# Kernel tuning notes

Measured on AMD Instinct MI355X. Metric: run time of the kernel, lower is better.

## Reference

```python
import jax, jax.numpy as jnp
import numpy as np

N_NODES = 50000
N_EDGES = 1_600_000
IN_DIM = 128
OUT_DIM = 128


def setup_inputs() -> dict:
    key = jax.random.key(0)
    k1, k2, k3, k4, k5, k6 = jax.random.split(key, 6)
    H = jax.random.normal(k1, (N_NODES, IN_DIM), dtype=jnp.float32)
    edge_src = jax.random.randint(k2, (N_EDGES,), 0, N_NODES, dtype=jnp.int32)
    edge_dst = jnp.sort(jax.random.randint(k3, (N_EDGES,), 0, N_NODES, dtype=jnp.int32))
    edge_weight = jax.random.uniform(k4, (N_EDGES,), dtype=jnp.float32)
    bound = np.sqrt(6.0 / (IN_DIM + OUT_DIM))
    W = jax.random.uniform(k5, (IN_DIM, OUT_DIM), dtype=jnp.float32, minval=-bound, maxval=bound)
    b = jax.random.normal(k6, (OUT_DIM,), dtype=jnp.float32)
    return {"H": H, "edge_src": edge_src, "edge_dst": edge_dst,
            "edge_weight": edge_weight, "W": W, "b": b}


def reference(H, edge_src, edge_dst, edge_weight, W, b):
    # A_hat @ H: gather source features, scale by edge weight, scatter-sum to dst.
    msgs = edge_weight[:, None] * jnp.take(H, edge_src, axis=0)   # [E, in_dim]
    agg = jax.ops.segment_sum(msgs, edge_dst, num_segments=N_NODES)  # [N, in_dim]
    # Dense transform + bias (no activation in original forward).
    return agg @ W + b
```

## Files before the change

### kernel.cpp

```cpp
#include <hip/hip_runtime.h>

#define IN_DIM 128
#define OUT_DIM 128

typedef __attribute__((ext_vector_type(8))) short short8v;
typedef __attribute__((ext_vector_type(4))) float float4v;
typedef __attribute__((ext_vector_type(4))) unsigned int uint4v;

__device__ __forceinline__ ushort f2bf(float f) {
    unsigned int u = __builtin_bit_cast(unsigned int, f);
    unsigned int r = (u + 0x7fffu + ((u >> 16) & 1u)) >> 16;
    return (ushort)r;
}

__device__ __forceinline__ unsigned int pk2bf(float x, float y) {
#if __has_builtin(__builtin_amdgcn_cvt_pk_bf16_f32)
    typedef __attribute__((ext_vector_type(2))) __bf16 bf2;
    bf2 r = __builtin_amdgcn_cvt_pk_bf16_f32(x, y);
    return __builtin_bit_cast(unsigned int, r);
#else
    return (unsigned int)f2bf(x) | ((unsigned int)f2bf(y) << 16);
#endif
}

__global__ __launch_bounds__(256) void prep_kernel(const float* __restrict__ W,
                                                   ushort* __restrict__ Wt) {
    int k0 = blockIdx.x * 8;
    int n = threadIdx.x & 127;
    int half = threadIdx.x >> 7;
#pragma unroll
    for (int kp = 0; kp < 2; ++kp) {
        int k = k0 + (half * 2 + kp) * 2;
        float v0 = W[k * 128 + n];
        float v1 = W[(k + 1) * 128 + n];
        *(unsigned int*)&Wt[n * 136 + k] = pk2bf(v0, v1);
    }
}

__global__ __launch_bounds__(256) void gemm_kernel(const float* __restrict__ H,
                                                   const ushort* __restrict__ Wt_g,
                                                   unsigned char* __restrict__ T8,
                                                   float* __restrict__ S, int M,
                                                   const int* __restrict__ edst,
                                                   int* __restrict__ rp,
                                                   int E, int nb_gemm) {
    __shared__ ushort Ws[128 * 136];

    const int t = threadIdx.x;

    if (blockIdx.x >= nb_gemm) {
        int n = (blockIdx.x - nb_gemm) * 256 + t;
        if (n <= M) {
            int lo = 0, hi = E;
            while (lo < hi) {
                int mid = (lo + hi) >> 1;
                if (edst[mid] < n) lo = mid + 1; else hi = mid;
            }
            rp[n] = lo;
        }
        return;
    }

    const int row0 = blockIdx.x * 64;

#pragma unroll
    for (int f = t; f < 2176; f += 256)
        ((short8v*)Ws)[f] = ((const short8v*)Wt_g)[f];

    const int w = t >> 6;
    const int l = t & 63;
    const int m16 = l & 15;
    const int kq = (l >> 4) * 8;
    const int gr = row0 + w * 16 + m16;

    float4 h[8];
    if (gr < M) {
#pragma unroll
        for (int ks = 0; ks < 4; ++ks) {
            h[ks * 2]     = *(const float4*)&H[gr * 128 + ks * 32 + kq];
            h[ks * 2 + 1] = *(const float4*)&H[gr * 128 + ks * 32 + kq + 4];
        }
    } else {
#pragma unroll
        for (int i = 0; i < 8; ++i) h[i] = make_float4(0.f, 0.f, 0.f, 0.f);
    }

    short8v bfrag[4];
#pragma unroll
    for (int ks = 0; ks < 4; ++ks) {
        uint4v u;
        u[0] = pk2bf(h[ks * 2].x, h[ks * 2].y);
        u[1] = pk2bf(h[ks * 2].z, h[ks * 2].w);
        u[2] = pk2bf(h[ks * 2 + 1].x, h[ks * 2 + 1].y);
        u[3] = pk2bf(h[ks * 2 + 1].z, h[ks * 2 + 1].w);
        bfrag[ks] = __builtin_bit_cast(short8v, u);
    }

    __syncthreads();

    float4v acc[8];
#pragma unroll
    for (int nt = 0; nt < 8; ++nt) acc[nt] = (float4v){0.f, 0.f, 0.f, 0.f};

#pragma unroll
    for (int ks = 0; ks < 4; ++ks) {
#pragma unroll
        for (int nt = 0; nt < 8; ++nt) {
            short8v afrag = *(const short8v*)&Ws[(nt * 16 + m16) * 136 + ks * 32 + kq];
            acc[nt] = __builtin_amdgcn_mfma_f32_16x16x32_bf16(afrag, bfrag[ks], acc[nt], 0, 0, 0);
        }
    }

    float mx = 0.f;
#pragma unroll
    for (int nt = 0; nt < 8; ++nt) {
#pragma unroll
        for (int k = 0; k < 4; ++k) mx = fmaxf(mx, fabsf(acc[nt][k]));
    }
    mx = fmaxf(mx, __shfl_xor(mx, 16));
    mx = fmaxf(mx, __shfl_xor(mx, 32));

    const float inv = 127.0f / fmaxf(mx, 1e-20f);

    if (gr < M) {
        const int qd = l >> 4;
        if (qd == 0) S[gr] = mx * (1.0f / 127.0f);
#pragma unroll
        for (int nt = 0; nt < 8; ++nt) {
            unsigned int p = 0;
#pragma unroll
            for (int k = 0; k < 4; ++k) {
                int qi = (int)__builtin_rintf(acc[nt][k] * inv);
                qi = qi > 127 ? 127 : (qi < -127 ? -127 : qi);
                p |= ((unsigned int)qi & 0xffu) << (k * 8);
            }
            *(unsigned int*)&T8[gr * 128 + nt * 16 + qd * 4] = p;
        }
    }
}

__global__ __launch_bounds__(256) void scatter_kernel(const ushort* __restrict__ T16,
                                                      const float* __restrict__ S,
                                                      const int* __restrict__ esrc,
                                                      const float* __restrict__ ew,
                                                      const int* __restrict__ rp,
                                                      const float* __restrict__ b,
                                                      float* __restrict__ out) {
    const int node = blockIdx.x * 4 + (threadIdx.x >> 6);
    const int lane = threadIdx.x & 63;
    const int col = lane << 1;

    const int s = rp[node];
    const int e = rp[node + 1];

    float2 bias = *(const float2*)&b[col];
    float ax = bias.x, ay = bias.y;

    for (int c = s; c < e; c += 64) {
        int idx = c + lane;
        int srcl = 0;
        float wl = 0.f;
        if (idx < e) { srcl = esrc[idx]; wl = ew[idx]; }
        int wli = __builtin_bit_cast(int, wl);
        int nn = e - c;
        if (nn > 64) nn = 64;

        for (int j = 0; j < nn; j += 8) {
            int ss[8];
            float ws[8];
            ushort vv[8];
#pragma unroll
            for (int q = 0; q < 8; ++q) {
                ss[q] = __builtin_amdgcn_readlane(srcl, j + q);
                float wq = __builtin_bit_cast(float, __builtin_amdgcn_readlane(wli, j + q));
                ws[q] = wq * S[ss[q]];
            }
#pragma unroll
            for (int q = 0; q < 8; ++q)
                vv[q] = T16[(unsigned int)ss[q] * 64u + (unsigned int)lane];
#pragma unroll
            for (int q = 0; q < 8; ++q) {
                int lo8 = (int)(signed char)(vv[q] & 0xff);
                int hi8 = (int)(signed char)(vv[q] >> 8);
                ax += ws[q] * (float)lo8;
                ay += ws[q] * (float)hi8;
            }
        }
    }

    *(float2*)&out[node * 128 + col] = make_float2(ax, ay);
}

extern "C" void kernel_launch(void* const* d_in, const int* in_sizes, int n_in,
                              void* d_out, int out_size, void* d_ws, size_t ws_size,
                              hipStream_t stream) {
    const float* H    = (const float*)d_in[0];
    const int*   esrc = (const int*)d_in[1];
    const int*   edst = (const int*)d_in[2];
    const float* ew   = (const float*)d_in[3];
    const float* W    = (const float*)d_in[4];
    const float* b    = (const float*)d_in[5];
    float* out = (float*)d_out;

    const int M = in_sizes[0] / IN_DIM;
    const int E = in_sizes[1];

    unsigned char* T8 = (unsigned char*)d_ws;
    size_t off = (size_t)M * 128;
    float* S  = (float*)((char*)d_ws + off);
    off += (size_t)M * 4;
    ushort* Wt = (ushort*)((char*)d_ws + off);
    off += 128 * 136 * 2;
    int* rp = (int*)((char*)d_ws + off);

    prep_kernel<<<16, 256, 0, stream>>>(W, Wt);

    const int nb_gemm = (M + 63) / 64;
    const int nb_rp   = (M + 1 + 255) / 256;
    gemm_kernel<<<nb_gemm + nb_rp, 256, 0, stream>>>(H, Wt, T8, S, M, edst, rp, E, nb_gemm);

    scatter_kernel<<<(M + 3) / 4, 256, 0, stream>>>((const ushort*)T8, S, esrc, ew, rp, b, out);
}
```

Baseline: 144.1 us.

## Store transformed features as fp16 instead of int8 with per-row scales

The GEMM output is now stored as packed fp16 rather than int8 with a per-row scale array, which removes the row max reduction and quantization in the GEMM epilogue and the scale lookups in the scatter kernel. The scatter kernel is also restructured: it drops the wave-cooperative edge loading with readlane broadcast and loads edge indices and weights directly with uniform (readfirstlane) bounds, unrolled by 8. The cost is twice the gather traffic per edge from the intermediate table. In exchange, accuracy is better than int8.

```diff
diff --git a/kernel.cpp b/kernel.cpp
--- a/kernel.cpp
+++ b/kernel.cpp
@@ -6,6 +6,8 @@
 typedef __attribute__((ext_vector_type(8))) short short8v;
 typedef __attribute__((ext_vector_type(4))) float float4v;
 typedef __attribute__((ext_vector_type(4))) unsigned int uint4v;
+typedef __attribute__((ext_vector_type(2))) unsigned int uint2v;
+typedef __attribute__((ext_vector_type(2))) __fp16 half2v;
 
 __device__ __forceinline__ ushort f2bf(float f) {
     unsigned int u = __builtin_bit_cast(unsigned int, f);
@@ -21,6 +23,11 @@
 #else
     return (unsigned int)f2bf(x) | ((unsigned int)f2bf(y) << 16);
 #endif
+}
+
+__device__ __forceinline__ unsigned int pk2f16(float x, float y) {
+    half2v r = __builtin_amdgcn_cvt_pkrtz(x, y);
+    return __builtin_bit_cast(unsigned int, r);
 }
 
 __global__ __launch_bounds__(256) void prep_kernel(const float* __restrict__ W,
@@ -39,8 +46,8 @@
 
 __global__ __launch_bounds__(256) void gemm_kernel(const float* __restrict__ H,
                                                    const ushort* __restrict__ Wt_g,
-                                                   unsigned char* __restrict__ T8,
-                                                   float* __restrict__ S, int M,
+                                                   __fp16* __restrict__ T,
+                                                   int M,
                                                    const int* __restrict__ edst,
                                                    int* __restrict__ rp,
                                                    int E, int nb_gemm) {
@@ -111,36 +118,18 @@
         }
     }
 
-    float mx = 0.f;
-#pragma unroll
-    for (int nt = 0; nt < 8; ++nt) {
-#pragma unroll
-        for (int k = 0; k < 4; ++k) mx = fmaxf(mx, fabsf(acc[nt][k]));
-    }
-    mx = fmaxf(mx, __shfl_xor(mx, 16));
-    mx = fmaxf(mx, __shfl_xor(mx, 32));
-
-    const float inv = 127.0f / fmaxf(mx, 1e-20f);
-
     if (gr < M) {
         const int qd = l >> 4;
-        if (qd == 0) S[gr] = mx * (1.0f / 127.0f);
 #pragma unroll
         for (int nt = 0; nt < 8; ++nt) {
-            unsigned int p = 0;
-#pragma unroll
-            for (int k = 0; k < 4; ++k) {
-                int qi = (int)__builtin_rintf(acc[nt][k] * inv);
-                qi = qi > 127 ? 127 : (qi < -127 ? -127 : qi);
-                p |= ((unsigned int)qi & 0xffu) << (k * 8);
-            }
-            *(unsigned int*)&T8[gr * 128 + nt * 16 + qd * 4] = p;
+            unsigned int u0 = pk2f16(acc[nt][0], acc[nt][1]);
+            unsigned int u1 = pk2f16(acc[nt][2], acc[nt][3]);
+            *(uint2v*)&T[gr * 128 + nt * 16 + qd * 4] = (uint2v){u0, u1};
         }
     }
 }
 
-__global__ __launch_bounds__(256) void scatter_kernel(const ushort* __restrict__ T16,
-                                                      const float* __restrict__ S,
+__global__ __launch_bounds__(256) void scatter_kernel(const __fp16* __restrict__ T,
                                                       const int* __restrict__ esrc,
                                                       const float* __restrict__ ew,
                                                       const int* __restrict__ rp,
@@ -148,47 +137,35 @@
                                                       float* __restrict__ out) {
     const int node = blockIdx.x * 4 + (threadIdx.x >> 6);
     const int lane = threadIdx.x & 63;
-    const int col = lane << 1;
 
-    const int s = rp[node];
-    const int e = rp[node + 1];
+    const int s = __builtin_amdgcn_readfirstlane(rp[node]);
+    const int e = __builtin_amdgcn_readfirstlane(rp[node + 1]);
 
-    float2 bias = *(const float2*)&b[col];
+    float2 bias = *(const float2*)&b[lane * 2];
     float ax = bias.x, ay = bias.y;
 
-    for (int c = s; c < e; c += 64) {
-        int idx = c + lane;
-        int srcl = 0;
-        float wl = 0.f;
-        if (idx < e) { srcl = esrc[idx]; wl = ew[idx]; }
-        int wli = __builtin_bit_cast(int, wl);
-        int nn = e - c;
-        if (nn > 64) nn = 64;
+    const unsigned int lo = (unsigned int)(lane * 2);
 
-        for (int j = 0; j < nn; j += 8) {
-            int ss[8];
-            float ws[8];
-            ushort vv[8];
+    int c = s;
+    for (; c + 8 <= e; c += 8) {
 #pragma unroll
-            for (int q = 0; q < 8; ++q) {
-                ss[q] = __builtin_amdgcn_readlane(srcl, j + q);
-                float wq = __builtin_bit_cast(float, __builtin_amdgcn_readlane(wli, j + q));
-                ws[q] = wq * S[ss[q]];
-            }
-#pragma unroll
-            for (int q = 0; q < 8; ++q)
-                vv[q] = T16[(unsigned int)ss[q] * 64u + (unsigned int)lane];
-#pragma unroll
-            for (int q = 0; q < 8; ++q) {
-                int lo8 = (int)(signed char)(vv[q] & 0xff);
-                int hi8 = (int)(signed char)(vv[q] >> 8);
-                ax += ws[q] * (float)lo8;
-                ay += ws[q] * (float)hi8;
-            }
+        for (int q = 0; q < 8; ++q) {
+            const int   sq = esrc[c + q];
+            const float wq = ew[c + q];
+            half2v h = *(const half2v*)&T[(unsigned int)sq * 128u + lo];
+            ax = fmaf((float)h.x, wq, ax);
+            ay = fmaf((float)h.y, wq, ay);
         }
     }
+    for (; c < e; ++c) {
+        const int   sq = esrc[c];
+        const float wq = ew[c];
+        half2v h = *(const half2v*)&T[(unsigned int)sq * 128u + lo];
+        ax = fmaf((float)h.x, wq, ax);
+        ay = fmaf((float)h.y, wq, ay);
+    }
 
-    *(float2*)&out[node * 128 + col] = make_float2(ax, ay);
+    *(float2*)&out[node * 128 + lane * 2] = make_float2(ax, ay);
 }
 
 extern "C" void kernel_launch(void* const* d_in, const int* in_sizes, int n_in,
@@ -205,10 +182,8 @@
     const int M = in_sizes[0] / IN_DIM;
     const int E = in_sizes[1];
 
-    unsigned char* T8 = (unsigned char*)d_ws;
-    size_t off = (size_t)M * 128;
-    float* S  = (float*)((char*)d_ws + off);
-    off += (size_t)M * 4;
+    __fp16* T = (__fp16*)d_ws;
+    size_t off = (size_t)M * 128 * 2;
     ushort* Wt = (ushort*)((char*)d_ws + off);
     off += 128 * 136 * 2;
     int* rp = (int*)((char*)d_ws + off);
@@ -217,7 +192,7 @@
 
     const int nb_gemm = (M + 63) / 64;
     const int nb_rp   = (M + 1 + 255) / 256;
-    gemm_kernel<<<nb_gemm + nb_rp, 256, 0, stream>>>(H, Wt, T8, S, M, edst, rp, E, nb_gemm);
+    gemm_kernel<<<nb_gemm + nb_rp, 256, 0, stream>>>(H, Wt, T, M, edst, rp, E, nb_gemm);
 
-    scatter_kernel<<<(M + 3) / 4, 256, 0, stream>>>((const ushort*)T8, S, esrc, ew, rp, b, out);
+    scatter_kernel<<<(M + 3) / 4, 256, 0, stream>>>(T, esrc, ew, rp, b, out);
 }
```

Measured after the change: 152.9 us. +6.1%, slower.
